# Kernel tuning notes

Hardware: AMD Instinct MI355X
Metric: run time of the kernel (lower is better)

The kernel has to match this reference:

```python
import jax, jax.numpy as jnp
import numpy as np
from jax import lax

TOP_K = 2

def _unfold(x_img, k):
    # F.unfold(kernel=k, stride=k): [B,C,H,W] -> [B, C*k*k, L], column index c*k*k + kh*k + kw
    B, C, H, W = x_img.shape
    Hp, Wp = H // k, W // k
    u = x_img.reshape(B, C, Hp, k, Wp, k).transpose(0, 1, 3, 5, 2, 4)
    return u.reshape(B, C * k * k, Hp * Wp)

def _fold(p, k, H, W):
    # F.fold inverse of non-overlapping unfold: [B, C*k*k, L] -> [B,C,H,W]
    B = p.shape[0]
    C = p.shape[1] // (k * k)
    Hp, Wp = H // k, W // k
    u = p.reshape(B, C, k, k, Hp, Wp).transpose(0, 1, 4, 2, 5, 3)
    return u.reshape(B, C, H, W)

def setup_inputs() -> dict:
    key = jax.random.key(0)
    ks = jax.random.split(key, 6)
    B, H, W, C, F, E, P = 8, 64, 64, 384, 1536, 8, 4
    N = H * W
    x = jax.random.normal(ks[0], (B, N, C), dtype=jnp.float32)
    gate_w = jax.random.normal(ks[1], (E, C, P, P), dtype=jnp.float32) * 0.01
    w1 = jax.random.normal(ks[2], (E, C, F), dtype=jnp.float32) * (1.0 / np.sqrt(C))
    b1 = jax.random.normal(ks[3], (E, F), dtype=jnp.float32) * 0.01
    w2 = jax.random.normal(ks[4], (E, F, C), dtype=jnp.float32) * (1.0 / np.sqrt(F))
    b2 = jax.random.normal(ks[5], (E, C), dtype=jnp.float32) * 0.01
    return {"x": x, "gate_w": gate_w, "w1": w1, "b1": b1, "w2": w2, "b2": b2, "H": H, "W": W}

def reference(x, gate_w, w1, b1, w2, b2, H, W):
    B, N, C = x.shape
    E, _, P, _ = gate_w.shape
    k2 = P * P
    Hp, Wp = H // P, W // P
    L = Hp * Wp
    x_img = jnp.transpose(x, (0, 2, 1)).reshape(B, C, H, W)
    # router: strided conv -> logits per patch
    logits_map = lax.conv_general_dilated(
        x_img, gate_w, window_strides=(P, P), padding='VALID',
        dimension_numbers=('NCHW', 'OIHW', 'NCHW'))  # [B,E,Hp,Wp]
    router_logits = jnp.transpose(logits_map, (0, 2, 3, 1)).reshape(B, L, E)
    probs = jax.nn.softmax(router_logits, axis=-1)
    ew, ei = lax.top_k(probs, TOP_K)  # [B,L,topk]
    ew = ew / (jnp.sum(ew, axis=-1, keepdims=True) + 1e-9)
    # expand to token level (faithful to original's reshape/flatten ordering)
    ei_tok = jnp.broadcast_to(ei[:, :, None, :], (B, L, k2, TOP_K)).reshape(-1, TOP_K)
    ew_tok = jnp.broadcast_to(ew[:, :, None, :], (B, L, k2, TOP_K)).reshape(-1, TOP_K)
    # unfold + the original's (scrambled) reshape(B, C, L, k2)
    U = _unfold(x_img, P)  # [B, C*k2, L]
    x_patches = jnp.transpose(U.reshape(B, C, L, k2), (0, 2, 3, 1))  # [B,L,k2,C]
    flat_x = x_patches.reshape(-1, C)  # [T,C], T = B*L*k2
    # combine weights: zero for experts not in top-k == masked dispatch math
    cw = jnp.zeros((flat_x.shape[0], E), dtype=flat_x.dtype)
    for kk in range(TOP_K):
        cw = cw + jax.nn.one_hot(ei_tok[:, kk], E, dtype=flat_x.dtype) * ew_tok[:, kk:kk + 1]
    out = jnp.zeros_like(flat_x)
    for e in range(E):
        h = jax.nn.gelu(flat_x @ w1[e] + b1[e], approximate=False)
        y = h @ w2[e] + b2[e]
        out = out + cw[:, e:e + 1] * y
    # fold back (mirrors original's reshape/permute exactly)
    o = jnp.transpose(out.reshape(B, L, k2, C), (0, 3, 1, 2)).reshape(B, C * k2, L)
    out_img = _fold(o, P, H, W)  # [B,C,H,W]
    # original: output.transpose(1,2).reshape(B,N,C) on NCHW tensor
    output = jnp.transpose(out_img, (0, 2, 1, 3)).reshape(B, N, C)
    return output
```

## Files before the change

kernel.cpp:

```cpp
#include <hip/hip_runtime.h>
#include <hip/hip_bf16.h>

#define BB   8
#define HH   64
#define WWID 64
#define CC   384
#define FF   1536
#define EE   8
#define LL   256
#define MTOTMAX 66560
#define NTMAX   520

typedef unsigned short ushort_t;
typedef __attribute__((ext_vector_type(4))) unsigned short u16x4;
typedef __attribute__((ext_vector_type(8))) short          s16x8;
typedef __attribute__((ext_vector_type(4))) float          f32x4;

__device__ __forceinline__ float bf2f(ushort_t u) {
  union { unsigned int i; float f; } v; v.i = ((unsigned int)u) << 16; return v.f;
}
__device__ __forceinline__ ushort_t f2bf(float f) {
  union { float f; unsigned int i; } v; v.f = f;
  unsigned int u = v.i;
  u += 0x7fffu + ((u >> 16) & 1u);
  return (ushort_t)(u >> 16);
}
__device__ __forceinline__ float gelu_f(float x) {
  float x2 = x * x;
  float t  = __builtin_fmaf(x2, -0.10294325f, -2.3022082f);
  float e  = __builtin_amdgcn_exp2f(x * t);
  float r  = __builtin_amdgcn_rcpf(1.0f + e);
  return x * r;
}

#define GLDS(g, l) __builtin_amdgcn_global_load_lds( \
    (const __attribute__((address_space(1))) void*)(g), \
    (__attribute__((address_space(3))) void*)(l), 16, 0, 0)

__global__ __launch_bounds__(256) void k_transpose(const float* __restrict__ src,
                                                   ushort_t* __restrict__ dst,
                                                   int R, int Cd) {
  __shared__ ushort_t tile[32][33];
  int e  = blockIdx.z;
  int c0 = blockIdx.x * 32, r0 = blockIdx.y * 32;
  int tx = threadIdx.x & 31, ty = threadIdx.x >> 5;
  const float* s = src + (size_t)e * R * Cd;
  ushort_t*    d = dst + (size_t)e * R * Cd;
  #pragma unroll
  for (int i = 0; i < 32; i += 8)
    tile[ty + i][tx] = f2bf(s[(size_t)(r0 + ty + i) * Cd + c0 + tx]);
  __syncthreads();
  #pragma unroll
  for (int i = 0; i < 32; i += 8)
    d[(size_t)(c0 + ty + i) * R + r0 + tx] = tile[tx][ty + i];
}

__global__ void k_tgw(const float* __restrict__ gw, float* __restrict__ gwt) {
  int e = blockIdx.x, t = threadIdx.x;
  for (int i = t; i < CC * 16; i += 256) {
    int c = i >> 4, p = i & 15;
    gwt[((size_t)e * 16 + p) * CC + c] = gw[(size_t)e * CC * 16 + i];
  }
}

__global__ __launch_bounds__(256) void k_router(const float* __restrict__ x,
                                                const float* __restrict__ gwt,
                                                int* __restrict__ re, float* __restrict__ rw,
                                                int* __restrict__ cnt) {
  int bid = blockIdx.x;
  int b = bid >> 8, l2 = bid & 255;
  int hp = l2 >> 4, wp = l2 & 15;
  int t = threadIdx.x;
  int e = t >> 5, lane = t & 31;
  const float* xb = x + (size_t)b * (HH * WWID) * CC;
  const float* ge = gwt + (size_t)e * 16 * CC;
  float acc = 0.f;
  #pragma unroll
  for (int p = 0; p < 16; ++p) {
    int pix = (hp * 4 + (p >> 2)) * 64 + wp * 4 + (p & 3);
    const float* xr = xb + (size_t)pix * CC;
    const float* gr = ge + (size_t)p * CC;
    #pragma unroll
    for (int it = 0; it < 3; ++it) {
      f32x4 xv = *reinterpret_cast<const f32x4*>(xr + it * 128 + lane * 4);
      f32x4 gv = *reinterpret_cast<const f32x4*>(gr + it * 128 + lane * 4);
      acc += xv.x * gv.x + xv.y * gv.y + xv.z * gv.z + xv.w * gv.w;
    }
  }
  #pragma unroll
  for (int d = 16; d; d >>= 1) acc += __shfl_down(acc, d, 32);
  __shared__ float logits[EE];
  if (lane == 0) logits[e] = acc;
  __syncthreads();
  if (t == 0) {
    float m = logits[0];
    #pragma unroll
    for (int i = 1; i < EE; ++i) m = fmaxf(m, logits[i]);
    float p[EE]; float s = 0.f;
    #pragma unroll
    for (int i = 0; i < EE; ++i) { p[i] = __expf(logits[i] - m); s += p[i]; }
    #pragma unroll
    for (int i = 0; i < EE; ++i) p[i] /= s;
    int e0 = 0;
    #pragma unroll
    for (int i = 1; i < EE; ++i) if (p[i] > p[e0]) e0 = i;
    int e1 = (e0 == 0) ? 1 : 0;
    #pragma unroll
    for (int i = 0; i < EE; ++i) if (i != e0 && p[i] > p[e1]) e1 = i;
    float s2 = p[e0] + p[e1] + 1e-9f;
    re[bid * 2 + 0] = e0;  re[bid * 2 + 1] = e1;
    rw[bid * 2 + 0] = p[e0] / s2;  rw[bid * 2 + 1] = p[e1] / s2;
    atomicAdd(&cnt[e0], 16);
    atomicAdd(&cnt[e1], 16);
  }
}

__global__ void k_pad(const int* __restrict__ cnt, int* __restrict__ cntp,
                      int* __restrict__ basep, int* __restrict__ tile2e,
                      int* __restrict__ gids, float* __restrict__ gwts) {
  __shared__ int s_cnt[EE], s_cntp[EE], s_base[EE + 1];
  int t = threadIdx.x;
  if (t == 0) {
    int b = 0;
    for (int e = 0; e < EE; ++e) {
      int c  = cnt[e];
      int cp = (c + 127) & ~127;
      s_cnt[e] = c; s_cntp[e] = cp; s_base[e] = b;
      b += cp;
    }
    s_base[EE] = b;
  }
  __syncthreads();
  if (t < EE) { cntp[t] = s_cntp[t]; basep[t] = s_base[t]; }
  if (t == EE) basep[EE] = s_base[EE];
  int ntot = s_base[EE] >> 7;
  for (int g = t; g < ntot; g += 256) {
    int e = 0;
    #pragma unroll
    for (int i = 1; i < EE; ++i) if (g * 128 >= s_base[i]) e = i;
    tile2e[g] = e;
  }
  for (int e = 0; e < EE; ++e)
    for (int i = s_cnt[e] + t; i < s_cntp[e]; i += 256) {
      gids[s_base[e] + i] = -1;
      gwts[s_base[e] + i] = 0.f;
    }
}

__global__ void k_assign(const int* __restrict__ re, const float* __restrict__ rw,
                         const int* __restrict__ basep, int* __restrict__ cnt2,
                         int* __restrict__ gids, float* __restrict__ gwts,
                         int* __restrict__ inv) {
  int i = blockIdx.x * blockDim.x + threadIdx.x;
  if (i >= BB * LL * 2) return;
  int pat = i >> 1, slot = i & 1;
  int b = pat >> 8, l2 = pat & 255;
  int e = re[i];
  float w = rw[i];
  int t2 = l2 >> 4, hp = l2 & 15;
  int kh = t2 >> 2, kw = t2 & 3;
  int h = hp * 4 + kh;
  int row = basep[e] + atomicAdd(&cnt2[e], 16);
  #pragma unroll
  for (int j = 0; j < 16; ++j) {
    int wpix = j * 4 + kw;
    int pix = (b << 12) + (h << 6) + wpix;
    gids[row + j] = pix;
    gwts[row + j] = w;
    inv[(slot << 15) + pix] = row + j;
  }
}

__global__ __launch_bounds__(256) void k_gather(const float* __restrict__ x,
                                                const int* __restrict__ gids,
                                                const int* __restrict__ basep,
                                                ushort_t* __restrict__ Xc, int t0) {
  int g = t0 + blockIdx.x;
  if (g * 128 >= basep[EE]) return;
  __shared__ int s_id[128];
  int t = threadIdx.x;
  if (t < 128) s_id[t] = gids[g * 128 + t];
  __syncthreads();
  ushort_t* dst = Xc + (size_t)blockIdx.x * 128 * CC;
  for (int i = t; i < 128 * 96; i += 256) {
    int row = i / 96, ch = (i % 96) * 4;
    int id = s_id[row];
    f32x4 v = (f32x4){0.f, 0.f, 0.f, 0.f};
    if (id >= 0) v = *reinterpret_cast<const f32x4*>(x + (size_t)(id & 32767) * CC + ch);
    u16x4 o = {f2bf(v.x), f2bf(v.y), f2bf(v.z), f2bf(v.w)};
    *reinterpret_cast<u16x4*>(dst + (size_t)row * CC + ch) = o;
  }
}

#define STAGE(DST, KOFF)                                                      \
  { _Pragma("unroll")                                                         \
    for (int c = 0; c < 4; ++c)                                               \
      GLDS(src_c[c] + (KOFF), (DST) + (w * 4 + c) * 512); }

#define PHASE(VM, RD, DOST, STDST, KOFF)                                      \
  {                                                                           \
    asm volatile("s_waitcnt vmcnt(" VM ")" ::: "memory");                     \
    __builtin_amdgcn_s_barrier();                                             \
    asm volatile("" ::: "memory");                                            \
    __builtin_amdgcn_sched_barrier(0);                                        \
    s16x8 af[4], bf[4];                                                       \
    _Pragma("unroll")                                                         \
    for (int i = 0; i < 4; ++i)                                               \
      af[i] = *reinterpret_cast<const s16x8*>((RD) + ((w & 1) * 4 + i) * 512 + lane * 8); \
    _Pragma("unroll")                                                         \
    for (int j = 0; j < 4; ++j)                                               \
      bf[j] = *reinterpret_cast<const s16x8*>((RD) + (8 + (w >> 1) * 4 + j) * 512 + lane * 8); \
    asm volatile("s_waitcnt lgkmcnt(0)" ::: "memory");                        \
    __builtin_amdgcn_sched_barrier(0);                                        \
    __builtin_amdgcn_s_barrier();                                             \
    asm volatile("" ::: "memory");                                            \
    if (DOST) STAGE(STDST, KOFF);                                             \
    __builtin_amdgcn_s_setprio(1);                                            \
    _Pragma("unroll")                                                         \
    for (int i = 0; i < 4; ++i)                                               \
      _Pragma("unroll")                                                       \
      for (int j = 0; j < 4; ++j)                                             \
        acc[i][j] = __builtin_amdgcn_mfma_f32_16x16x32_bf16(af[i], bf[j], acc[i][j], 0, 0, 0); \
    __builtin_amdgcn_s_setprio(0);                                            \
  }

template<int K, int NOUT, bool GELU, bool OUTG>
__global__ __launch_bounds__(256, 4) void k_gemm(const ushort_t* __restrict__ A,
                                                 const ushort_t* __restrict__ Bsrc,
                                                 const float* __restrict__ bias,
                                                 const int* __restrict__ basep,
                                                 const int* __restrict__ tile2e,
                                                 const float* __restrict__ gwts,
                                                 ushort_t* __restrict__ out, int t0) {
  constexpr int NX = NOUT / 128;
  int nwg = NX * (int)gridDim.y;
  int wg  = (int)blockIdx.y * NX + (int)blockIdx.x;
  int id  = (wg & 7) * (nwg >> 3) + (wg >> 3);
  int ng  = id % NX;
  int ly  = id / NX;
  int g   = t0 + ly;
  if (g * 128 >= basep[EE]) return;
  int e = tile2e[g];
  __shared__ ushort_t S[2][16 * 512];
  int t = threadIdx.x, w = t >> 6, lane = t & 63;
  int l15 = lane & 15, q = lane >> 4;
  const ushort_t* a_src = A + ((size_t)e * NOUT + ng * 128) * K;
  const ushort_t* b_src = Bsrc + (size_t)ly * 128 * K;

  const ushort_t* src_c[4];
  #pragma unroll
  for (int c = 0; c < 4; ++c) {
    int ch = w * 4 + c;
    src_c[c] = (ch < 8)
      ? a_src + (size_t)(ch * 16 + l15) * K + q * 8
      : b_src + (size_t)((ch - 8) * 16 + l15) * K + q * 8;
  }

  f32x4 acc[4][4];
  #pragma unroll
  for (int i = 0; i < 4; ++i)
    #pragma unroll
    for (int j = 0; j < 4; ++j) acc[i][j] = (f32x4){0.f, 0.f, 0.f, 0.f};

  ushort_t* S0v = &S[0][0];
  ushort_t* S1v = &S[1][0];

  STAGE(S0v, 0);
  STAGE(S1v, 32);

  constexpr int NIT = K / 32;
  for (int it = 0; it < NIT - 2; it += 2) {
    PHASE("4", S0v, true, S0v, (size_t)(it + 2) * 32);
    PHASE("4", S1v, true, S1v, (size_t)(it + 3) * 32);
  }
  PHASE("4", S0v, false, S0v, 0);
  PHASE("0", S1v, false, S1v, 0);

  int nb = ng * 128 + (w & 1) * 64 + q * 4;
  f32x4 bv[4];
  #pragma unroll
  for (int i = 0; i < 4; ++i)
    bv[i] = *reinterpret_cast<const f32x4*>(bias + (size_t)e * NOUT + nb + i * 16);
  ushort_t* ob = out + (OUTG ? (size_t)g : (size_t)ly) * 128 * NOUT;
  #pragma unroll
  for (int j = 0; j < 4; ++j) {
    int m = (w >> 1) * 64 + j * 16 + l15;
    float wt = GELU ? 1.f : gwts[g * 128 + m];
    ushort_t* op = ob + (size_t)m * NOUT + nb;
    #pragma unroll
    for (int i = 0; i < 4; ++i) {
      u16x4 v;
      #pragma unroll
      for (int r = 0; r < 4; ++r) {
        float xv = acc[i][j][r] + bv[i][r];
        v[r] = f2bf(GELU ? gelu_f(xv) : xv * wt);
      }
      *reinterpret_cast<u16x4*>(op + i * 16) = v;
    }
  }
}

__global__ __launch_bounds__(256) void k_final(const ushort_t* __restrict__ y,
                                               const int* __restrict__ inv,
                                               float* __restrict__ out) {
  int bid = blockIdx.x;
  __shared__ float tile[64][193];
  __shared__ int s_r0[64], s_r1[64];
  int t = threadIdx.x;
  if (t < 64) {
    s_r0[t] = inv[(bid << 6) + t];
    s_r1[t] = inv[32768 + (bid << 6) + t];
  }
  __syncthreads();
  float* dst = out + (size_t)bid * CC * WWID;
  #pragma unroll
  for (int half = 0; half < 2; ++half) {
    int c0 = half * 192;
    for (int i = t; i < 64 * 48; i += 256) {
      int w = i / 48, c4 = (i % 48) * 4;
      u16x4 a = *reinterpret_cast<const u16x4*>(y + (size_t)s_r0[w] * CC + c0 + c4);
      u16x4 b = *reinterpret_cast<const u16x4*>(y + (size_t)s_r1[w] * CC + c0 + c4);
      #pragma unroll
      for (int k = 0; k < 4; ++k)
        tile[w][c4 + k] = bf2f(a[k]) + bf2f(b[k]);
    }
    __syncthreads();
    for (int i = t; i < 64 * 192; i += 256) {
      int cl = i / 64, w = i % 64;
      dst[(size_t)(c0 + cl) * WWID + w] = tile[w][cl];
    }
    __syncthreads();
  }
}

extern "C" void kernel_launch(void* const* d_in, const int* in_sizes, int n_in,
                              void* d_out, int out_size, void* d_ws, size_t ws_size,
                              hipStream_t stream) {
  const float* x  = (const float*)d_in[0];
  const float* gw = (const float*)d_in[1];
  const float* w1 = (const float*)d_in[2];
  const float* b1 = (const float*)d_in[3];
  const float* w2 = (const float*)d_in[4];
  const float* b2 = (const float*)d_in[5];

  const size_t fixed = (size_t)EE * FF * CC * 2 * 2
                     + (size_t)MTOTMAX * CC * 2
                     + (size_t)EE * 16 * CC * 4
                     + (size_t)MTOTMAX * 4 * 2
                     + (size_t)65536 * 4
                     + (size_t)BB * LL * 2 * 4 * 2
                     + (size_t)NTMAX * 4
                     + 1024;
  const int cands[6] = {32768, 16384, 8192, 4096, 2048, 1024};
  int MC = 1024;
  for (int i = 0; i < 6; ++i)
    if (fixed + (size_t)cands[i] * 3840 <= ws_size) { MC = cands[i]; break; }
  const int npass = (MTOTMAX + MC - 1) / MC;
  const int ntile = MC / 128;

  char* ws = (char*)d_ws;
  size_t off = 0;
  ushort_t* Xc   = (ushort_t*)(ws + off); off += (size_t)MC * CC * 2;
  ushort_t* Hc   = (ushort_t*)(ws + off); off += (size_t)MC * FF * 2;
  ushort_t* w1t  = (ushort_t*)(ws + off); off += (size_t)EE * FF * CC * 2;
  ushort_t* w2t  = (ushort_t*)(ws + off); off += (size_t)EE * FF * CC * 2;
  ushort_t* y    = (ushort_t*)(ws + off); off += (size_t)MTOTMAX * CC * 2;
  float* gwt   = (float*)(ws + off); off += (size_t)EE * 16 * CC * 4;
  int*   gids  = (int*)(ws + off);   off += (size_t)MTOTMAX * 4;
  float* gwts  = (float*)(ws + off); off += (size_t)MTOTMAX * 4;
  int*   inv   = (int*)(ws + off);   off += (size_t)65536 * 4;
  int*   re    = (int*)(ws + off);   off += (size_t)BB * LL * 2 * 4;
  float* rw    = (float*)(ws + off); off += (size_t)BB * LL * 2 * 4;
  int*   tile2e= (int*)(ws + off);   off += (size_t)NTMAX * 4;
  int*   cnt   = (int*)(ws + off);   off += 64;
  int*   cnt2  = (int*)(ws + off);   off += 64;
  int*   cntp  = (int*)(ws + off);   off += 64;
  int*   basep = (int*)(ws + off);   off += 64;

  hipMemsetAsync(cnt, 0, 128, stream);

  k_transpose<<<dim3(FF / 32, CC / 32, EE), 256, 0, stream>>>(w1, w1t, CC, FF);
  k_transpose<<<dim3(CC / 32, FF / 32, EE), 256, 0, stream>>>(w2, w2t, FF, CC);
  k_tgw<<<EE, 256, 0, stream>>>(gw, gwt);
  k_router<<<BB * LL, 256, 0, stream>>>(x, gwt, re, rw, cnt);
  k_pad<<<1, 256, 0, stream>>>(cnt, cntp, basep, tile2e, gids, gwts);
  k_assign<<<16, 256, 0, stream>>>(re, rw, basep, cnt2, gids, gwts, inv);

  for (int p = 0; p < npass; ++p) {
    int t0 = p * ntile;
    k_gather<<<ntile, 256, 0, stream>>>(x, gids, basep, Xc, t0);
    k_gemm<CC, FF, true,  false><<<dim3(FF / 128, ntile), 256, 0, stream>>>(
        w1t, Xc, b1, basep, tile2e, (const float*)nullptr, Hc, t0);
    k_gemm<FF, CC, false, true ><<<dim3(CC / 128, ntile), 256, 0, stream>>>(
        w2t, Hc, b2, basep, tile2e, gwts, y, t0);
  }
  k_final<<<BB * HH, 256, 0, stream>>>(y, inv, (float*)d_out);
}
```

Baseline: 678.6 us.

## Replace LDS-staged GEMM operand loads with direct register double-buffered global loads

```diff
diff --git a/kernel.cpp b/kernel.cpp
--- a/kernel.cpp
+++ b/kernel.cpp
@@ -32,10 +32,6 @@
   float r  = __builtin_amdgcn_rcpf(1.0f + e);
   return x * r;
 }
-
-#define GLDS(g, l) __builtin_amdgcn_global_load_lds( \
-    (const __attribute__((address_space(1))) void*)(g), \
-    (__attribute__((address_space(3))) void*)(l), 16, 0, 0)
 
 __global__ __launch_bounds__(256) void k_transpose(const float* __restrict__ src,
                                                    ushort_t* __restrict__ dst,
@@ -192,40 +188,25 @@
   }
 }
 
-#define STAGE(DST, KOFF)                                                      \
+#define LOADAB(AF, BF, KO)                                                    \
   { _Pragma("unroll")                                                         \
-    for (int c = 0; c < 4; ++c)                                               \
-      GLDS(src_c[c] + (KOFF), (DST) + (w * 4 + c) * 512); }
-
-#define PHASE(VM, RD, DOST, STDST, KOFF)                                      \
-  {                                                                           \
-    asm volatile("s_waitcnt vmcnt(" VM ")" ::: "memory");                     \
-    __builtin_amdgcn_s_barrier();                                             \
-    asm volatile("" ::: "memory");                                            \
-    __builtin_amdgcn_sched_barrier(0);                                        \
-    s16x8 af[4], bf[4];                                                       \
-    _Pragma("unroll")                                                         \
     for (int i = 0; i < 4; ++i)                                               \
-      af[i] = *reinterpret_cast<const s16x8*>((RD) + ((w & 1) * 4 + i) * 512 + lane * 8); \
+      AF[i] = *reinterpret_cast<const s16x8*>(a_lane + (size_t)i * 16 * K + (KO)); \
     _Pragma("unroll")                                                         \
     for (int j = 0; j < 4; ++j)                                               \
-      bf[j] = *reinterpret_cast<const s16x8*>((RD) + (8 + (w >> 1) * 4 + j) * 512 + lane * 8); \
-    asm volatile("s_waitcnt lgkmcnt(0)" ::: "memory");                        \
-    __builtin_amdgcn_sched_barrier(0);                                        \
-    __builtin_amdgcn_s_barrier();                                             \
-    asm volatile("" ::: "memory");                                            \
-    if (DOST) STAGE(STDST, KOFF);                                             \
-    __builtin_amdgcn_s_setprio(1);                                            \
+      BF[j] = *reinterpret_cast<const s16x8*>(b_lane + (size_t)j * 16 * K + (KO)); }
+
+#define MFMA16(AF, BF)                                                        \
+  { __builtin_amdgcn_s_setprio(1);                                            \
     _Pragma("unroll")                                                         \
     for (int i = 0; i < 4; ++i)                                               \
       _Pragma("unroll")                                                       \
       for (int j = 0; j < 4; ++j)                                             \
-        acc[i][j] = __builtin_amdgcn_mfma_f32_16x16x32_bf16(af[i], bf[j], acc[i][j], 0, 0, 0); \
-    __builtin_amdgcn_s_setprio(0);                                            \
-  }
+        acc[i][j] = __builtin_amdgcn_mfma_f32_16x16x32_bf16(AF[i], BF[j], acc[i][j], 0, 0, 0); \
+    __builtin_amdgcn_s_setprio(0); }
 
 template<int K, int NOUT, bool GELU, bool OUTG>
-__global__ __launch_bounds__(256, 4) void k_gemm(const ushort_t* __restrict__ A,
+__global__ __launch_bounds__(256, 3) void k_gemm(const ushort_t* __restrict__ A,
                                                  const ushort_t* __restrict__ Bsrc,
                                                  const float* __restrict__ bias,
                                                  const int* __restrict__ basep,
@@ -241,20 +222,12 @@
   int g   = t0 + ly;
   if (g * 128 >= basep[EE]) return;
   int e = tile2e[g];
-  __shared__ ushort_t S[2][16 * 512];
   int t = threadIdx.x, w = t >> 6, lane = t & 63;
   int l15 = lane & 15, q = lane >> 4;
   const ushort_t* a_src = A + ((size_t)e * NOUT + ng * 128) * K;
   const ushort_t* b_src = Bsrc + (size_t)ly * 128 * K;
-
-  const ushort_t* src_c[4];
-  #pragma unroll
-  for (int c = 0; c < 4; ++c) {
-    int ch = w * 4 + c;
-    src_c[c] = (ch < 8)
-      ? a_src + (size_t)(ch * 16 + l15) * K + q * 8
-      : b_src + (size_t)((ch - 8) * 16 + l15) * K + q * 8;
-  }
+  const ushort_t* a_lane = a_src + (size_t)((w & 1) * 64 + l15) * K + q * 8;
+  const ushort_t* b_lane = b_src + (size_t)((w >> 1) * 64 + l15) * K + q * 8;
 
   f32x4 acc[4][4];
   #pragma unroll
@@ -262,19 +235,16 @@
     #pragma unroll
     for (int j = 0; j < 4; ++j) acc[i][j] = (f32x4){0.f, 0.f, 0.f, 0.f};
 
-  ushort_t* S0v = &S[0][0];
-  ushort_t* S1v = &S[1][0];
-
-  STAGE(S0v, 0);
-  STAGE(S1v, 32);
-
+  s16x8 aC[4], bC[4], aN[4], bN[4];
   constexpr int NIT = K / 32;
-  for (int it = 0; it < NIT - 2; it += 2) {
-    PHASE("4", S0v, true, S0v, (size_t)(it + 2) * 32);
-    PHASE("4", S1v, true, S1v, (size_t)(it + 3) * 32);
-  }
-  PHASE("4", S0v, false, S0v, 0);
-  PHASE("0", S1v, false, S1v, 0);
+  LOADAB(aC, bC, 0);
+  for (int it = 0; it < NIT; it += 2) {
+    LOADAB(aN, bN, (it + 1) * 32);
+    MFMA16(aC, bC);
+    int k2 = (it + 2 < NIT) ? (it + 2) * 32 : 0;
+    LOADAB(aC, bC, k2);
+    MFMA16(aN, bN);
+  }
 
   int nb = ng * 128 + (w & 1) * 64 + q * 4;
   f32x4 bv[4];
```

Result: slower. 951.8 us (+40.3%).

## Enlarge expert GEMM tiles to 256-row blocks with 512-thread workgroups

Applied to the files above, without the earlier changes.

```diff
diff --git a/kernel.cpp b/kernel.cpp
--- a/kernel.cpp
+++ b/kernel.cpp
@@ -8,8 +8,8 @@
 #define FF   1536
 #define EE   8
 #define LL   256
-#define MTOTMAX 66560
-#define NTMAX   520
+#define MTOTMAX 67584
+#define NTMAX   264
 
 typedef unsigned short ushort_t;
 typedef __attribute__((ext_vector_type(4))) unsigned short u16x4;
@@ -124,7 +124,7 @@
     int b = 0;
     for (int e = 0; e < EE; ++e) {
       int c  = cnt[e];
-      int cp = (c + 127) & ~127;
+      int cp = (c + 255) & ~255;
       s_cnt[e] = c; s_cntp[e] = cp; s_base[e] = b;
       b += cp;
     }
@@ -133,11 +133,11 @@
   __syncthreads();
   if (t < EE) { cntp[t] = s_cntp[t]; basep[t] = s_base[t]; }
   if (t == EE) basep[EE] = s_base[EE];
-  int ntot = s_base[EE] >> 7;
+  int ntot = s_base[EE] >> 8;
   for (int g = t; g < ntot; g += 256) {
     int e = 0;
     #pragma unroll
-    for (int i = 1; i < EE; ++i) if (g * 128 >= s_base[i]) e = i;
+    for (int i = 1; i < EE; ++i) if (g * 256 >= s_base[i]) e = i;
     tile2e[g] = e;
   }
   for (int e = 0; e < EE; ++e)
@@ -194,101 +194,108 @@
 
 #define STAGE(DST, KOFF)                                                      \
   { _Pragma("unroll")                                                         \
-    for (int c = 0; c < 4; ++c)                                               \
-      GLDS(src_c[c] + (KOFF), (DST) + (w * 4 + c) * 512); }
-
-#define PHASE(VM, RD, DOST, STDST, KOFF)                                      \
+    for (int c = 0; c < NC; ++c)                                              \
+      GLDS(src_c[c] + (KOFF), (DST) + (w * NC + c) * 512); }
+
+#define PHASE(VMFULL, RD, DOST, KOFF)                                         \
   {                                                                           \
-    asm volatile("s_waitcnt vmcnt(" VM ")" ::: "memory");                     \
+    if (VMFULL) {                                                             \
+      if constexpr (NC == 4) { asm volatile("s_waitcnt vmcnt(4)" ::: "memory"); } \
+      else                   { asm volatile("s_waitcnt vmcnt(3)" ::: "memory"); } \
+    } else {                                                                  \
+      asm volatile("s_waitcnt vmcnt(0)" ::: "memory");                        \
+    }                                                                         \
     __builtin_amdgcn_s_barrier();                                             \
-    asm volatile("" ::: "memory");                                            \
     __builtin_amdgcn_sched_barrier(0);                                        \
-    s16x8 af[4], bf[4];                                                       \
+    s16x8 af[FI], bf[4];                                                      \
     _Pragma("unroll")                                                         \
-    for (int i = 0; i < 4; ++i)                                               \
-      af[i] = *reinterpret_cast<const s16x8*>((RD) + ((w & 1) * 4 + i) * 512 + lane * 8); \
+    for (int i = 0; i < FI; ++i)                                              \
+      af[i] = *reinterpret_cast<const s16x8*>((RD) + (wf * FI + i) * 512 + lane * 8); \
     _Pragma("unroll")                                                         \
     for (int j = 0; j < 4; ++j)                                               \
-      bf[j] = *reinterpret_cast<const s16x8*>((RD) + (8 + (w >> 1) * 4 + j) * 512 + lane * 8); \
+      bf[j] = *reinterpret_cast<const s16x8*>((RD) + (2 * FI + wm * 4 + j) * 512 + lane * 8); \
     asm volatile("s_waitcnt lgkmcnt(0)" ::: "memory");                        \
     __builtin_amdgcn_sched_barrier(0);                                        \
     __builtin_amdgcn_s_barrier();                                             \
-    asm volatile("" ::: "memory");                                            \
-    if (DOST) STAGE(STDST, KOFF);                                             \
+    if (DOST) STAGE(RD, KOFF);                                                \
     __builtin_amdgcn_s_setprio(1);                                            \
     _Pragma("unroll")                                                         \
-    for (int i = 0; i < 4; ++i)                                               \
+    for (int i = 0; i < FI; ++i)                                              \
       _Pragma("unroll")                                                       \
       for (int j = 0; j < 4; ++j)                                             \
         acc[i][j] = __builtin_amdgcn_mfma_f32_16x16x32_bf16(af[i], bf[j], acc[i][j], 0, 0, 0); \
     __builtin_amdgcn_s_setprio(0);                                            \
   }
 
-template<int K, int NOUT, bool GELU, bool OUTG>
-__global__ __launch_bounds__(256, 4) void k_gemm(const ushort_t* __restrict__ A,
+template<int K, int NOUT, int TN, bool GELU, bool OUTG>
+__global__ __launch_bounds__(512, 2) void k_gemm(const ushort_t* __restrict__ A,
                                                  const ushort_t* __restrict__ Bsrc,
                                                  const float* __restrict__ bias,
                                                  const int* __restrict__ basep,
                                                  const int* __restrict__ tile2e,
                                                  const float* __restrict__ gwts,
                                                  ushort_t* __restrict__ out, int t0) {
-  constexpr int NX = NOUT / 128;
+  constexpr int FI  = TN / 32;
+  constexpr int NCH = 2 * FI + 16;
+  constexpr int NC  = NCH / 8;
+  constexpr int NX  = NOUT / TN;
   int nwg = NX * (int)gridDim.y;
   int wg  = (int)blockIdx.y * NX + (int)blockIdx.x;
-  int id  = (wg & 7) * (nwg >> 3) + (wg >> 3);
+  int id  = ((nwg & 7) == 0) ? ((wg & 7) * (nwg >> 3) + (wg >> 3)) : wg;
   int ng  = id % NX;
   int ly  = id / NX;
   int g   = t0 + ly;
-  if (g * 128 >= basep[EE]) return;
+  if (g * 256 >= basep[EE]) return;
   int e = tile2e[g];
-  __shared__ ushort_t S[2][16 * 512];
+  __shared__ ushort_t S[2][NCH * 512];
   int t = threadIdx.x, w = t >> 6, lane = t & 63;
   int l15 = lane & 15, q = lane >> 4;
-  const ushort_t* a_src = A + ((size_t)e * NOUT + ng * 128) * K;
-  const ushort_t* b_src = Bsrc + (size_t)ly * 128 * K;
-
-  const ushort_t* src_c[4];
-  #pragma unroll
-  for (int c = 0; c < 4; ++c) {
-    int ch = w * 4 + c;
-    src_c[c] = (ch < 8)
+  int wf = w & 1, wm = w >> 1;
+  const ushort_t* a_src = A + ((size_t)e * NOUT + ng * TN) * K;
+  const ushort_t* b_src = Bsrc + (size_t)ly * 256 * K;
+
+  const ushort_t* src_c[NC];
+  #pragma unroll
+  for (int c = 0; c < NC; ++c) {
+    int ch = w * NC + c;
+    src_c[c] = (ch < 2 * FI)
       ? a_src + (size_t)(ch * 16 + l15) * K + q * 8
-      : b_src + (size_t)((ch - 8) * 16 + l15) * K + q * 8;
-  }
-
-  f32x4 acc[4][4];
-  #pragma unroll
-  for (int i = 0; i < 4; ++i)
+      : b_src + (size_t)((ch - 2 * FI) * 16 + l15) * K + q * 8;
+  }
+
+  f32x4 acc[FI][4];
+  #pragma unroll
+  for (int i = 0; i < FI; ++i)
     #pragma unroll
     for (int j = 0; j < 4; ++j) acc[i][j] = (f32x4){0.f, 0.f, 0.f, 0.f};
 
-  ushort_t* S0v = &S[0][0];
-  ushort_t* S1v = &S[1][0];
-
-  STAGE(S0v, 0);
-  STAGE(S1v, 32);
+  ushort_t* S0 = &S[0][0];
+  ushort_t* S1 = &S[1][0];
+
+  STAGE(S0, 0);
+  STAGE(S1, 32);
 
   constexpr int NIT = K / 32;
   for (int it = 0; it < NIT - 2; it += 2) {
-    PHASE("4", S0v, true, S0v, (size_t)(it + 2) * 32);
-    PHASE("4", S1v, true, S1v, (size_t)(it + 3) * 32);
-  }
-  PHASE("4", S0v, false, S0v, 0);
-  PHASE("0", S1v, false, S1v, 0);
-
-  int nb = ng * 128 + (w & 1) * 64 + q * 4;
-  f32x4 bv[4];
-  #pragma unroll
-  for (int i = 0; i < 4; ++i)
+    PHASE(true, S0, true, (size_t)(it + 2) * 32);
+    PHASE(true, S1, true, (size_t)(it + 3) * 32);
+  }
+  PHASE(true,  S0, false, 0);
+  PHASE(false, S1, false, 0);
+
+  int nb = ng * TN + wf * (TN / 2) + q * 4;
+  f32x4 bv[FI];
+  #pragma unroll
+  for (int i = 0; i < FI; ++i)
     bv[i] = *reinterpret_cast<const f32x4*>(bias + (size_t)e * NOUT + nb + i * 16);
-  ushort_t* ob = out + (OUTG ? (size_t)g : (size_t)ly) * 128 * NOUT;
+  ushort_t* ob = out + (OUTG ? (size_t)g : (size_t)ly) * 256 * NOUT;
   #pragma unroll
   for (int j = 0; j < 4; ++j) {
-    int m = (w >> 1) * 64 + j * 16 + l15;
-    float wt = GELU ? 1.f : gwts[g * 128 + m];
+    int m = wm * 64 + j * 16 + l15;
+    float wt = GELU ? 1.f : gwts[g * 256 + m];
     ushort_t* op = ob + (size_t)m * NOUT + nb;
     #pragma unroll
-    for (int i = 0; i < 4; ++i) {
+    for (int i = 0; i < FI; ++i) {
       u16x4 v;
       #pragma unroll
       for (int r = 0; r < 4; ++r) {
@@ -356,7 +363,8 @@
   for (int i = 0; i < 6; ++i)
     if (fixed + (size_t)cands[i] * 3840 <= ws_size) { MC = cands[i]; break; }
   const int npass = (MTOTMAX + MC - 1) / MC;
-  const int ntile = MC / 128;
+  const int nt128 = MC / 128;
+  const int nt256 = MC / 256;
 
   char* ws = (char*)d_ws;
   size_t off = 0;
@@ -387,12 +395,11 @@
   k_assign<<<16, 256, 0, stream>>>(re, rw, basep, cnt2, gids, gwts, inv);
 
   for (int p = 0; p < npass; ++p) {
-    int t0 = p * ntile;
-    k_gather<<<ntile, 256, 0, stream>>>(x, gids, basep, Xc, t0);
-    k_gemm<CC, FF, true,  false><<<dim3(FF / 128, ntile), 256, 0, stream>>>(
-        w1t, Xc, b1, basep, tile2e, (const float*)nullptr, Hc, t0);
-    k_gemm<FF, CC, false, true ><<<dim3(CC / 128, ntile), 256, 0, stream>>>(
-        w2t, Hc, b2, basep, tile2e, gwts, y, t0);
+    k_gather<<<nt128, 256, 0, stream>>>(x, gids, basep, Xc, p * nt128);
+    k_gemm<CC, FF, 256, true,  false><<<dim3(FF / 256, nt256), 512, 0, stream>>>(
+        w1t, Xc, b1, basep, tile2e, (const float*)nullptr, Hc, p * nt256);
+    k_gemm<FF, CC, 128, false, true ><<<dim3(CC / 128, nt256), 512, 0, stream>>>(
+        w2t, Hc, b2, basep, tile2e, gwts, y, p * nt256);
   }
   k_final<<<BB * HH, 256, 0, stream>>>(y, inv, (float*)d_out);
 }
```

Result: faster. 655.1 us (-3.5%).
